# Kernel tuning notes

Measured on AMD Instinct MI355X. Metric: run time of the kernel, lower is better.

## Reference

```python
import jax, jax.numpy as jnp
import numpy as np

V = 30000   # vocab (len(en_dict))
D = 256     # embed/d_model
H = 4       # heads
DK = D // H
N = 1024    # max_len
B = 16      # batch
HID = 256   # ffn hidden
NEG = -1e10
SCALE = 1.0 / np.sqrt(DK)


def setup_inputs() -> dict:
    key = jax.random.key(0)
    ks = jax.random.split(key, 24)
    g = lambda i, shape, s=0.02: jax.random.normal(ks[i], shape, jnp.float32) * s
    return {
        'input_ids': jax.random.randint(ks[0], (B, N), 0, V),
        'attention_mask': jnp.ones((B, N), jnp.int32),
        'emb_W': g(1, (D, V)), 'emb_b': g(2, (D,)),
        'wq': g(3, (D, D)), 'bq': g(4, (D,)),
        'wk': g(5, (D, D)), 'bk': g(6, (D,)),
        'wv': g(7, (D, D)), 'bv': g(8, (D,)),
        'fc_w': g(9, (D, D)), 'fc_b': g(10, (D,)),
        'ff_w1': g(11, (HID, D)), 'ff_b1': g(12, (HID,)),
        'ff_w2': g(13, (D, HID)), 'ff_b2': g(14, (D,)),
        'h1_w': g(15, (128, D)), 'h1_b': g(16, (128,)),
        'bn_gamma': jnp.ones((128,)), 'bn_beta': jnp.zeros((128,)),
        'bn_mean': jnp.zeros((128,)), 'bn_var': jnp.ones((128,)),
        'h2_w': g(17, (1, 128)), 'h2_b': g(18, (1,)),
    }


def _pos_encoding():
    pos = jnp.arange(N, dtype=jnp.float32)[:, None]
    down = jnp.exp(jnp.arange(0, D, 2, dtype=jnp.float32) * (-np.log(10000.0) / D))
    ang = pos * down  # (N, D/2)
    pe = jnp.zeros((N, D), jnp.float32)
    pe = pe.at[:, 0::2].set(jnp.sin(ang) / 10.0)
    pe = pe.at[:, 1::2].set(jnp.cos(ang) / 10.0)
    return pe


def _forward(input_ids, attention_mask, emb_W, emb_b, wq, bq, wk, bk, wv, bv,
             fc_w, fc_b, ff_w1, ff_b1, ff_w2, ff_b2, h1_w, h1_b,
             bn_gamma, bn_beta, bn_mean, bn_var, h2_w, h2_b):
    # one-hot @ W^T + b  ==  direct column gather of W
    x = emb_W.T[input_ids] + emb_b          # (B, N, D)
    x = x + _pos_encoding()                  # dropout off (eval)

    # --- multi-head self-attention with per-sample span mask ---
    def heads(w, b):
        return (jnp.einsum('bnd,ed->bne', x, w) + b).reshape(B, N, H, DK).transpose(0, 2, 1, 3)
    q, k, v = heads(wq, bq), heads(wk, bk), heads(wv, bv)
    scores = jnp.einsum('bhnd,bhmd->bhnm', q, k) * SCALE  # (B,H,N,N)

    m = attention_mask.astype(bool)
    start = jnp.argmax(m, axis=1)                    # first True
    end = N - 1 - jnp.argmax(m[:, ::-1], axis=1)     # last True (exclusive end in slice)
    idx = jnp.arange(N)
    in_span = (idx[None, :] >= start[:, None]) & (idx[None, :] < end[:, None])  # (B,N)
    allowed = in_span[:, :, None] & in_span[:, None, :]                         # (B,N,N)
    scores = scores + jnp.where(allowed, 0.0, NEG)[:, None, :, :]

    p = jax.nn.softmax(scores, axis=-1)
    att = jnp.einsum('bhnm,bhmd->bhnd', p, v).transpose(0, 2, 1, 3).reshape(B, N, D)
    att = jnp.einsum('bnd,ed->bne', att, fc_w) + fc_b
    x = x + att

    # --- feed-forward (replaces x, no residual; dropout off; exact GELU) ---
    h = jax.nn.gelu(jnp.einsum('bnd,hd->bnh', x, ff_w1) + ff_b1, approximate=False)
    x = jnp.einsum('bnh,dh->bnd', h, ff_w2) + ff_b2

    # --- mean pool + MLP head (BatchNorm in eval mode) ---
    pooled = jnp.mean(x, axis=1)                      # (B, D)
    h = pooled @ h1_w.T + h1_b                        # (B, 128)
    h = (h - bn_mean) / jnp.sqrt(bn_var + 1e-5) * bn_gamma + bn_beta
    h = jax.nn.relu(h)
    return h @ h2_w.T + h2_b                          # (B, 1)


def reference(input_ids, attention_mask, emb_W, emb_b, wq, bq, wk, bk, wv, bv,
              fc_w, fc_b, ff_w1, ff_b1, ff_w2, ff_b2, h1_w, h1_b,
              bn_gamma, bn_beta, bn_mean, bn_var, h2_w, h2_b):
    return _forward(input_ids, attention_mask, emb_W, emb_b, wq, bq, wk, bk, wv, bv,
                    fc_w, fc_b, ff_w1, ff_b1, ff_w2, ff_b2, h1_w, h1_b,
                    bn_gamma, bn_beta, bn_mean, bn_var, h2_w, h2_b)
```

## Files before the change

kernel.cpp:

```cpp
#include <hip/hip_runtime.h>
#include <math.h>

#define VOCAB 30000
#define DMODEL 256
#define NHEAD 4
#define SEQ 1024
#define BATCH 16
#define MROWS (BATCH*SEQ)
#define SL2 0.18033688011112042f
#define NEG2 (-1.4426950408889634e10f)

typedef __attribute__((ext_vector_type(8))) short bf16x8;
typedef __attribute__((ext_vector_type(4))) float f32x4;

#if __has_builtin(__builtin_amdgcn_exp2f)
#define EXP2F __builtin_amdgcn_exp2f
#else
#define EXP2F exp2f
#endif

__device__ __forceinline__ unsigned short f2b(float f) {
    unsigned int u = __float_as_uint(f);
    unsigned int r = (u + 0x7FFFu + ((u >> 16) & 1u)) >> 16;
    return (unsigned short)r;
}
__device__ __forceinline__ unsigned short f2b_trunc(float f) {
    return (unsigned short)(__float_as_uint(f) >> 16);
}
__device__ __forceinline__ float b2f(unsigned short s) {
    unsigned int u = ((unsigned int)s) << 16;
    return __uint_as_float(u);
}

__global__ __launch_bounds__(256) void prep_kernel(const int* __restrict__ mask, int* __restrict__ spans,
                                                   float* __restrict__ pe,
                                                   const float* __restrict__ wq, const float* __restrict__ wk,
                                                   const float* __restrict__ wv, const float* __restrict__ bq,
                                                   const float* __restrict__ bk, const float* __restrict__ bv,
                                                   unsigned short* __restrict__ wqkv, float* __restrict__ bias768,
                                                   const float* __restrict__ fcw, const float* __restrict__ f1w,
                                                   const float* __restrict__ f2w, unsigned short* __restrict__ wb3,
                                                   const float* __restrict__ embW, const float* __restrict__ eb,
                                                   unsigned short* __restrict__ embT) {
    int blk = blockIdx.x;
    int t = threadIdx.x;
    if (blk < 64) {
        __shared__ double down[128];
        if (t < 128) down[t] = exp((double)(2 * t) * (-9.210340371976184 / 256.0));
        __syncthreads();
        int d2 = t & 127, half = t >> 7;
        #pragma unroll
        for (int i = 0; i < 8; i++) {
            int n = blk * 16 + half * 8 + i;
            double ang = (double)n * down[d2];
            pe[n * DMODEL + 2 * d2]     = (float)(sin(ang) * 0.1);
            pe[n * DMODEL + 2 * d2 + 1] = (float)(cos(ang) * 0.1);
        }
    } else if (blk < 80) {
        int b = blk - 64;
        __shared__ int smin, smax;
        if (t == 0) { smin = SEQ; smax = -1; }
        __syncthreads();
        int lmin = SEQ, lmax = -1;
        for (int i = t; i < SEQ; i += 256) {
            if (mask[b * SEQ + i] != 0) { lmin = min(lmin, i); lmax = max(lmax, i); }
        }
        atomicMin(&smin, lmin);
        atomicMax(&smax, lmax);
        __syncthreads();
        if (t == 0) {
            int st, en;
            if (smax < 0) { st = 0; en = SEQ - 1; }
            else          { st = smin; en = smax; }
            spans[b * 2] = st; spans[b * 2 + 1] = en;
        }
    } else if (blk < 849) {
        int cb = blk - 80;
        if (cb < 768) {
            const float* src = (cb < 256) ? wq : (cb < 512) ? wk : wv;
            wqkv[cb * 256 + t] = f2b(src[(cb & 255) * 256 + t]);
        } else {
            for (int j = t; j < 768; j += 256)
                bias768[j] = (j < 256) ? bq[j] : (j < 512) ? bk[j - 256] : bv[j - 512];
        }
    } else if (blk < 1617) {
        int cb = blk - 849;
        const float* src = (cb < 256) ? fcw : (cb < 512) ? f1w : f2w;
        wb3[cb * 256 + t] = f2b(src[(cb & 255) * 256 + t]);
    } else {
        __shared__ float tsh[32][33];
        int tb = blk - 1617;
        int bx = tb % 938, by = tb / 938;
        int tx = t & 31, ty = t >> 5;
        int c0 = bx * 32, r0 = by * 32;
        for (int i = 0; i < 32; i += 8) {
            int r = r0 + ty + i, c = c0 + tx;
            if (c < VOCAB) tsh[ty + i][tx] = embW[(size_t)r * VOCAB + c];
        }
        __syncthreads();
        float ebv = eb[r0 + tx];
        for (int i = 0; i < 32; i += 8) {
            int c = c0 + ty + i, r = r0 + tx;
            if (c < VOCAB) embT[(size_t)c * DMODEL + r] = f2b(tsh[tx][ty + i] + ebv);
        }
    }
}

__global__ void embed_kernel(const int* __restrict__ ids, const unsigned short* __restrict__ embT,
                             const float* __restrict__ pe, unsigned short* __restrict__ x0b) {
    int bn = blockIdx.x;
    int d = threadIdx.x;
    int id = ids[bn];
    int n = bn & (SEQ - 1);
    float v = b2f(embT[(size_t)id * DMODEL + d]) + pe[n * DMODEL + d];
    x0b[(size_t)bn * DMODEL + d] = f2b(v);
}

__global__ __launch_bounds__(512) void qkv_kernel(const unsigned short* __restrict__ A,
                                                  const unsigned short* __restrict__ W,
                                                  const float* __restrict__ bias,
                                                  unsigned short* __restrict__ Qb,
                                                  unsigned short* __restrict__ Kb,
                                                  unsigned short* __restrict__ Vt) {
    __shared__ unsigned short XA[4 * 64 * 64];
    __shared__ unsigned short Bs[2][256 * 64];
    int tid = threadIdx.x;
    int m0 = blockIdx.x * 64;
    int w = tid >> 6, l = tid & 63;
    int wrow = w >> 1, wcol = w & 1;
    int lg = l >> 4, ll = l & 15;
    int bb = m0 >> 10;

    #pragma unroll
    for (int i = 0; i < 4; i++) {
        int s = tid + i * 512;
        int row = s >> 5;
        int kb = (s & 31) * 16;
        int kt = kb >> 7, within = kb & 127;
        int swz = within ^ ((row & 7) << 4);
        float4 av = *(const float4*)((const char*)A + (size_t)(m0 + row) * 512 + kb);
        *(float4*)((char*)XA + kt * 8192 + row * 128 + swz) = av;
    }

    for (int nb = 0; nb < 3; nb++) {
        f32x4 acc[8] = {};
        #pragma unroll
        for (int i = 0; i < 4; i++) {
            int s = tid + i * 512;
            int row = s >> 3, kb = (s & 7) * 16;
            int swz = kb ^ ((row & 7) << 4);
            float4 bv = *(const float4*)((const char*)W + (size_t)(nb * 256 + row) * 512 + kb);
            *(float4*)((char*)Bs[0] + row * 128 + swz) = bv;
        }
        __syncthreads();

        for (int kt = 0; kt < 4; kt++) {
            int cur = kt & 1;
            float4 pre[4];
            if (kt < 3) {
                #pragma unroll
                for (int i = 0; i < 4; i++) {
                    int s = tid + i * 512;
                    int row = s >> 3, kb = (s & 7) * 16;
                    pre[i] = *(const float4*)((const char*)W + (size_t)(nb * 256 + row) * 512 + (kt + 1) * 128 + kb);
                }
            }
            int arow = wrow * 16 + ll;
            bf16x8 af[2];
            #pragma unroll
            for (int ks = 0; ks < 2; ks++)
                af[ks] = *(const bf16x8*)((const char*)XA + kt * 8192 + arow * 128 + ((lg * 16 + ks * 64) ^ ((arow & 7) << 4)));
            #pragma unroll
            for (int nf = 0; nf < 8; nf++) {
                int brow = wcol * 128 + nf * 16 + ll;
                #pragma unroll
                for (int ks = 0; ks < 2; ks++) {
                    bf16x8 bf = *(const bf16x8*)((const char*)Bs[cur] + brow * 128 + ((lg * 16 + ks * 64) ^ ((brow & 7) << 4)));
                    acc[nf] = __builtin_amdgcn_mfma_f32_16x16x32_bf16(af[ks], bf, acc[nf], 0, 0, 0);
                }
            }
            if (kt < 3) {
                #pragma unroll
                for (int i = 0; i < 4; i++) {
                    int s = tid + i * 512;
                    int row = s >> 3, kb = (s & 7) * 16;
                    int swz = kb ^ ((row & 7) << 4);
                    *(float4*)((char*)Bs[cur ^ 1] + row * 128 + swz) = pre[i];
                }
            }
            __syncthreads();
        }
        #pragma unroll
        for (int nf = 0; nf < 8; nf++) {
            int col = wcol * 128 + nf * 16 + ll;
            float bv = bias[nb * 256 + col];
            int hh = col >> 6, dk = col & 63;
            if (nb == 2) {
                unsigned int lo = (unsigned int)f2b(acc[nf][0] + bv) | ((unsigned int)f2b(acc[nf][1] + bv) << 16);
                unsigned int hi = (unsigned int)f2b(acc[nf][2] + bv) | ((unsigned int)f2b(acc[nf][3] + bv) << 16);
                int ns = (m0 & 1023) + wrow * 16 + lg * 4;
                unsigned int* dst = (unsigned int*)(Vt + ((((size_t)bb * 4 + hh) * 64) + dk) * 1024 + ns);
                dst[0] = lo;
                dst[1] = hi;
            } else {
                #pragma unroll
                for (int r2 = 0; r2 < 4; r2++) {
                    int ns = (m0 & 1023) + wrow * 16 + lg * 4 + r2;
                    float v = acc[nf][r2] + bv;
                    if (nb == 0)
                        Qb[((((size_t)bb * 4 + hh) * 1024) + ns) * 64 + dk] = f2b(v * SL2);
                    else
                        Kb[((((size_t)bb * 4 + hh) * 1024) + ns) * 64 + dk] = f2b(v);
                }
            }
        }
    }
}

__global__ __launch_bounds__(512) void attn_coop(const unsigned short* __restrict__ Qb,
                                                 const unsigned short* __restrict__ Kb,
                                                 const unsigned short* __restrict__ Vt,
                                                 const int* __restrict__ spans,
                                                 unsigned short* __restrict__ attb) {
    __shared__ unsigned short Ks[2][64 * 64];
    __shared__ unsigned short Vs[2][64 * 64];
    __shared__ __align__(16) unsigned short Ps[8][16 * 72];
    int tid = threadIdx.x;
    int w = tid >> 6, l = tid & 63;
    int id = blockIdx.x;
    int c = id & 7, rest = id >> 3;
    int bh = c * 8 + (rest >> 3);
    int qg = rest & 7;
    int q0 = qg * 128 + w * 16;
    int b = bh >> 2, h = bh & 3;
    int lg = l >> 4, ll = l & 15;
    const char* Kp = (const char*)(Kb + (size_t)bh * SEQ * 64);
    const char* Vp = (const char*)(Vt + (size_t)bh * 64 * SEQ);
    const unsigned short* Qp = Qb + (size_t)bh * SEQ * 64;
    int start = spans[b * 2], end = spans[b * 2 + 1];

    bf16x8 qf[2];
    #pragma unroll
    for (int ks = 0; ks < 2; ks++)
        qf[ks] = *(const bf16x8*)(Qp + (size_t)(q0 + ll) * 64 + lg * 8 + ks * 32);

    bf16x8 ones;
    #pragma unroll
    for (int i = 0; i < 8; i++) ones[i] = (short)0x3F80;

    f32x4 o[4] = {};
    f32x4 accl = {};
    bool rowok[4];
    #pragma unroll
    for (int r2 = 0; r2 < 4; r2++) {
        int rr = q0 + lg * 4 + r2;
        rowok[r2] = (rr >= start) && (rr < end);
    }

    int srow = tid >> 3, skb = (tid & 7) * 16;
    int sswz = skb ^ ((srow & 7) << 4);

    {
        float4 kv0v = *(const float4*)(Kp + (size_t)srow * 128 + skb);
        float4 vv0 = *(const float4*)(Vp + (size_t)srow * 2048 + skb);
        *(float4*)((char*)Ks[0] + srow * 128 + sswz) = kv0v;
        *(float4*)((char*)Vs[0] + srow * 128 + sswz) = vv0;
    }

    for (int ct = 0; ct < 16; ct++) {
        int cur = ct & 1;
        int kv0 = ct * 64;
        __syncthreads();

        float4 kreg, vreg;
        if (ct < 15) {
            int kvn = kv0 + 64;
            kreg = *(const float4*)(Kp + (size_t)(kvn + srow) * 128 + skb);
            vreg = *(const float4*)(Vp + (size_t)srow * 2048 + kvn * 2 + skb);
        }

        f32x4 s4[4];
        #pragma unroll
        for (int nf = 0; nf < 4; nf++) {
            int cc = kv0 + nf * 16 + ll;
            float ci = ((cc >= start) && (cc < end)) ? 0.f : NEG2;
            f32x4 cv = { ci, ci, ci, ci };
            s4[nf] = cv;
        }
        #pragma unroll
        for (int ks = 0; ks < 2; ks++)
            #pragma unroll
            for (int nf = 0; nf < 4; nf++) {
                int row = nf * 16 + ll;
                bf16x8 kf = *(const bf16x8*)((const char*)Ks[cur] + row * 128 + ((lg * 16 + ks * 64) ^ ((row & 7) << 4)));
                s4[nf] = __builtin_amdgcn_mfma_f32_16x16x32_bf16(qf[ks], kf, s4[nf], 0, 0, 0);
            }

        #pragma unroll
        for (int nf = 0; nf < 4; nf++)
            #pragma unroll
            for (int r2 = 0; r2 < 4; r2++) {
                float sv = rowok[r2] ? s4[nf][r2] : 0.f;
                s4[nf][r2] = EXP2F(sv);
            }

        #pragma unroll
        for (int nf = 0; nf < 4; nf++)
            #pragma unroll
            for (int r2 = 0; r2 < 4; r2++)
                Ps[w][(lg * 4 + r2) * 72 + nf * 16 + ll] = f2b_trunc(s4[nf][r2]);

        bf16x8 pa[2];
        #pragma unroll
        for (int ks = 0; ks < 2; ks++)
            pa[ks] = *(const bf16x8*)(&Ps[w][ll * 72 + lg * 8 + ks * 32]);

        #pragma unroll
        for (int ks = 0; ks < 2; ks++)
            #pragma unroll
            for (int cf = 0; cf < 4; cf++) {
                int row = cf * 16 + ll;
                bf16x8 vf = *(const bf16x8*)((const char*)Vs[cur] + row * 128 + ((lg * 16 + ks * 64) ^ ((row & 7) << 4)));
                o[cf] = __builtin_amdgcn_mfma_f32_16x16x32_bf16(pa[ks], vf, o[cf], 0, 0, 0);
            }
        #pragma unroll
        for (int ks = 0; ks < 2; ks++)
            accl = __builtin_amdgcn_mfma_f32_16x16x32_bf16(pa[ks], ones, accl, 0, 0, 0);

        if (ct < 15) {
            *(float4*)((char*)Ks[cur ^ 1] + srow * 128 + sswz) = kreg;
            *(float4*)((char*)Vs[cur ^ 1] + srow * 128 + sswz) = vreg;
        }
    }

    #pragma unroll
    for (int r2 = 0; r2 < 4; r2++) {
        float inv = 1.f / accl[r2];
        int row = q0 + lg * 4 + r2;
        #pragma unroll
        for (int cf = 0; cf < 4; cf++) {
            int dk = cf * 16 + ll;
            attb[((size_t)b * SEQ + row) * 256 + h * 64 + dk] = f2b(o[cf][r2] * inv);
        }
    }
}

__global__ __launch_bounds__(512) void ffn_kernel(const unsigned short* __restrict__ attb,
                                                  const unsigned short* __restrict__ x0b,
                                                  const unsigned short* __restrict__ W3,
                                                  const float* __restrict__ fcb,
                                                  const float* __restrict__ f1b,
                                                  const float* __restrict__ f2bv,
                                                  float* __restrict__ part) {
    __shared__ unsigned short BufA[4 * 64 * 64];
    __shared__ unsigned short BufB[4 * 64 * 64];
    __shared__ unsigned short Bs[2][256 * 64];
    int tid = threadIdx.x;
    int m0 = blockIdx.x * 64;
    int w = tid >> 6, l = tid & 63;
    int wrow = w >> 1, wcol = w & 1;
    int lg = l >> 4, ll = l & 15;
    int arow = wrow * 16 + ll;

    #pragma unroll
    for (int i = 0; i < 4; i++) {
        int s = tid + i * 512;
        int row = s >> 5;
        int kb = (s & 31) * 16;
        int kt = kb >> 7, within = kb & 127;
        int swz = within ^ ((row & 7) << 4);
        float4 av = *(const float4*)((const char*)attb + (size_t)(m0 + row) * 512 + kb);
        *(float4*)((char*)BufA + kt * 8192 + row * 128 + swz) = av;
    }

    #pragma unroll
    for (int phase = 0; phase < 3; phase++) {
        const unsigned short* Wp = W3 + phase * 65536;
        const char* Asrc = (phase == 1) ? (const char*)BufB : (const char*)BufA;
        f32x4 acc[8] = {};
        #pragma unroll
        for (int i = 0; i < 4; i++) {
            int s = tid + i * 512;
            int row = s >> 3, kb = (s & 7) * 16;
            int swz = kb ^ ((row & 7) << 4);
            float4 bv = *(const float4*)((const char*)Wp + (size_t)row * 512 + kb);
            *(float4*)((char*)Bs[0] + row * 128 + swz) = bv;
        }
        __syncthreads();

        for (int kt = 0; kt < 4; kt++) {
            int cur = kt & 1;
            float4 pre[4];
            if (kt < 3) {
                #pragma unroll
                for (int i = 0; i < 4; i++) {
                    int s = tid + i * 512;
                    int row = s >> 3, kb = (s & 7) * 16;
                    pre[i] = *(const float4*)((const char*)Wp + (size_t)row * 512 + (kt + 1) * 128 + kb);
                }
            }
            bf16x8 af[2];
            #pragma unroll
            for (int ks = 0; ks < 2; ks++)
                af[ks] = *(const bf16x8*)(Asrc + kt * 8192 + arow * 128 + ((lg * 16 + ks * 64) ^ ((arow & 7) << 4)));
            #pragma unroll
            for (int nf = 0; nf < 8; nf++) {
                int brow = wcol * 128 + nf * 16 + ll;
                #pragma unroll
                for (int ks = 0; ks < 2; ks++) {
                    bf16x8 bf = *(const bf16x8*)((const char*)Bs[cur] + brow * 128 + ((lg * 16 + ks * 64) ^ ((brow & 7) << 4)));
                    acc[nf] = __builtin_amdgcn_mfma_f32_16x16x32_bf16(af[ks], bf, acc[nf], 0, 0, 0);
                }
            }
            if (kt < 3) {
                #pragma unroll
                for (int i = 0; i < 4; i++) {
                    int s = tid + i * 512;
                    int row = s >> 3, kb = (s & 7) * 16;
                    int swz = kb ^ ((row & 7) << 4);
                    *(float4*)((char*)Bs[cur ^ 1] + row * 128 + swz) = pre[i];
                }
            }
            __syncthreads();
        }

        if (phase == 0) {
            #pragma unroll
            for (int nf = 0; nf < 8; nf++) {
                int col = wcol * 128 + nf * 16 + ll;
                float bv = fcb[col];
                int kt = col >> 6;
                int byteoff = (2 * (col & 63));
                #pragma unroll
                for (int r2 = 0; r2 < 4; r2++) {
                    int row = wrow * 16 + lg * 4 + r2;
                    *(unsigned short*)((char*)BufB + kt * 8192 + row * 128 + (byteoff ^ ((row & 7) << 4))) = f2b(acc[nf][r2] + bv);
                }
            }
            __syncthreads();
            #pragma unroll
            for (int i = 0; i < 4; i++) {
                int s = tid + i * 512;
                int row = s >> 5;
                int kb = (s & 31) * 16;
                int kt = kb >> 7, within = kb & 127;
                int swz = within ^ ((row & 7) << 4);
                bf16x8* dst = (bf16x8*)((char*)BufB + kt * 8192 + row * 128 + swz);
                bf16x8 xv = *dst;
                bf16x8 rv = *(const bf16x8*)((const char*)x0b + (size_t)(m0 + row) * 512 + kb);
                bf16x8 res;
                #pragma unroll
                for (int jj = 0; jj < 8; jj++)
                    res[jj] = (short)f2b(b2f((unsigned short)xv[jj]) + b2f((unsigned short)rv[jj]));
                *dst = res;
            }
        } else if (phase == 1) {
            #pragma unroll
            for (int nf = 0; nf < 8; nf++) {
                int col = wcol * 128 + nf * 16 + ll;
                float bv = f1b[col];
                int kt = col >> 6;
                int byteoff = (2 * (col & 63));
                #pragma unroll
                for (int r2 = 0; r2 < 4; r2++) {
                    int row = wrow * 16 + lg * 4 + r2;
                    float v = acc[nf][r2] + bv;
                    v = 0.5f * v * (1.f + erff(v * 0.70710678118654752f));
                    *(unsigned short*)((char*)BufA + kt * 8192 + row * 128 + (byteoff ^ ((row & 7) << 4))) = f2b(v);
                }
            }
        } else {
            int bb = m0 >> 10;
            int chunk = ((m0 & 1023) >> 4) + wrow;
            #pragma unroll
            for (int nf = 0; nf < 8; nf++) {
                int col = wcol * 128 + nf * 16 + ll;
                float s_ = acc[nf][0] + acc[nf][1] + acc[nf][2] + acc[nf][3];
                s_ += __shfl_xor(s_, 16);
                s_ += __shfl_xor(s_, 32);
                s_ += 16.f * f2bv[col];
                if (lg == 0)
                    part[((size_t)bb * 64 + chunk) * 256 + col] = s_;
            }
        }
    }
}

__global__ __launch_bounds__(128) void head2_kernel(const float* __restrict__ part,
                                                    const float* __restrict__ h1_w, const float* __restrict__ h1_b,
                                                    const float* __restrict__ g, const float* __restrict__ be,
                                                    const float* __restrict__ mu, const float* __restrict__ var,
                                                    const float* __restrict__ h2_w, const float* __restrict__ h2_b,
                                                    float* __restrict__ out) {
    int b = blockIdx.x, j = threadIdx.x;
    __shared__ float pl[256];
    __shared__ float red[128];
    float s0 = 0.f, s1 = 0.f;
    for (int ch = 0; ch < 64; ch++) {
        s0 += part[((size_t)b * 64 + ch) * 256 + j];
        s1 += part[((size_t)b * 64 + ch) * 256 + j + 128];
    }
    pl[j] = s0 * (1.f / 1024.f);
    pl[j + 128] = s1 * (1.f / 1024.f);
    __syncthreads();
    float s = 0.f;
    for (int d = 0; d < 256; d++) s = fmaf(pl[d], h1_w[j * 256 + d], s);
    s += h1_b[j];
    s = (s - mu[j]) / sqrtf(var[j] + 1e-5f) * g[j] + be[j];
    s = fmaxf(s, 0.f);
    red[j] = s * h2_w[j];
    __syncthreads();
    for (int off = 64; off; off >>= 1) {
        if (j < off) red[j] += red[j + off];
        __syncthreads();
    }
    if (j == 0) out[b] = red[0] + h2_b[0];
}

extern "C" void kernel_launch(void* const* d_in, const int* in_sizes, int n_in,
                              void* d_out, int out_size, void* d_ws, size_t ws_size,
                              hipStream_t stream) {
    (void)in_sizes; (void)n_in; (void)out_size; (void)ws_size;
    const int*   ids    = (const int*)d_in[0];
    const int*   amask  = (const int*)d_in[1];
    const float* emb_W  = (const float*)d_in[2];
    const float* emb_b  = (const float*)d_in[3];
    const float* wq = (const float*)d_in[4],  *bq = (const float*)d_in[5];
    const float* wk = (const float*)d_in[6],  *bk = (const float*)d_in[7];
    const float* wv = (const float*)d_in[8],  *bv = (const float*)d_in[9];
    const float* fcw = (const float*)d_in[10], *fcb = (const float*)d_in[11];
    const float* f1w = (const float*)d_in[12], *f1b = (const float*)d_in[13];
    const float* f2w = (const float*)d_in[14], *f2b_ = (const float*)d_in[15];
    const float* h1w = (const float*)d_in[16], *h1b = (const float*)d_in[17];
    const float* bng = (const float*)d_in[18], *bnb = (const float*)d_in[19];
    const float* bnm = (const float*)d_in[20], *bnv = (const float*)d_in[21];
    const float* h2w = (const float*)d_in[22], *h2b = (const float*)d_in[23];
    float* out = (float*)d_out;
    float* ws = (float*)d_ws;

    const size_t O_PE   = 0;
    const size_t O_EMBT = O_PE + 262144;
    const size_t O_X0B  = O_EMBT + 3840000;
    const size_t O_Q    = O_X0B + 2097152;
    const size_t O_K    = O_Q + 2097152;
    const size_t O_V    = O_K + 2097152;
    const size_t O_ATT  = O_V + 2097152;
    const size_t O_WQKV = O_ATT + 2097152;
    const size_t O_WB3  = O_WQKV + 98304;
    const size_t O_B768 = O_WB3 + 98304;
    const size_t O_PART = O_B768 + 768;
    const size_t O_SPAN = O_PART + 262144;

    float* pe   = ws + O_PE;
    unsigned short* embT = (unsigned short*)(ws + O_EMBT);
    unsigned short* x0b  = (unsigned short*)(ws + O_X0B);
    unsigned short* Qb   = (unsigned short*)(ws + O_Q);
    unsigned short* Kb   = (unsigned short*)(ws + O_K);
    unsigned short* Vt   = (unsigned short*)(ws + O_V);
    unsigned short* attb = (unsigned short*)(ws + O_ATT);
    unsigned short* wqkv = (unsigned short*)(ws + O_WQKV);
    unsigned short* wb3  = (unsigned short*)(ws + O_WB3);
    float* bias768 = ws + O_B768;
    float* part = ws + O_PART;
    int* spans  = (int*)(ws + O_SPAN);

    prep_kernel<<<1617 + 938 * 8, 256, 0, stream>>>(amask, spans, pe,
                                                    wq, wk, wv, bq, bk, bv, wqkv, bias768,
                                                    fcw, f1w, f2w, wb3,
                                                    emb_W, emb_b, embT);
    embed_kernel<<<MROWS, 256, 0, stream>>>(ids, embT, pe, x0b);

    qkv_kernel<<<256, 512, 0, stream>>>(x0b, wqkv, bias768, Qb, Kb, Vt);

    attn_coop<<<512, 512, 0, stream>>>(Qb, Kb, Vt, spans, attb);

    ffn_kernel<<<256, 512, 0, stream>>>(attb, x0b, wb3, fcb, f1b, f2b_, part);

    head2_kernel<<<BATCH, 128, 0, stream>>>(part, h1w, h1b, bng, bnb, bnm, bnv, h2w, h2b, out);
}
```

Before: 100.1 us.

## Fuse embedding gather into QKV kernel and retile FFN to 32-row blocks

Removes the separate embed kernel by gathering embedding rows and adding positional encoding inside the QKV kernel's A-tile load, also writing x0b for the residual. The FFN kernel is retiled from 64-row to 32-row blocks with 4 column-warps, doubling the grid to 512 blocks, and drops the double-buffered weight tile in favour of a single buffer with extra barriers. This saves a launch and a round trip of x0b, and gives more FFN blocks for occupancy, at the cost of reloading the weights twice as often and losing load/compute overlap in the FFN.

```diff
diff --git a/kernel.cpp b/kernel.cpp
--- a/kernel.cpp
+++ b/kernel.cpp
@@ -106,19 +106,12 @@
     }
 }
 
-__global__ void embed_kernel(const int* __restrict__ ids, const unsigned short* __restrict__ embT,
-                             const float* __restrict__ pe, unsigned short* __restrict__ x0b) {
-    int bn = blockIdx.x;
-    int d = threadIdx.x;
-    int id = ids[bn];
-    int n = bn & (SEQ - 1);
-    float v = b2f(embT[(size_t)id * DMODEL + d]) + pe[n * DMODEL + d];
-    x0b[(size_t)bn * DMODEL + d] = f2b(v);
-}
-
-__global__ __launch_bounds__(512) void qkv_kernel(const unsigned short* __restrict__ A,
+__global__ __launch_bounds__(512) void qkv_kernel(const int* __restrict__ ids,
+                                                  const unsigned short* __restrict__ embT,
+                                                  const float* __restrict__ pe,
                                                   const unsigned short* __restrict__ W,
                                                   const float* __restrict__ bias,
+                                                  unsigned short* __restrict__ x0b,
                                                   unsigned short* __restrict__ Qb,
                                                   unsigned short* __restrict__ Kb,
                                                   unsigned short* __restrict__ Vt) {
@@ -138,8 +131,23 @@
         int kb = (s & 31) * 16;
         int kt = kb >> 7, within = kb & 127;
         int swz = within ^ ((row & 7) << 4);
-        float4 av = *(const float4*)((const char*)A + (size_t)(m0 + row) * 512 + kb);
-        *(float4*)((char*)XA + kt * 8192 + row * 128 + swz) = av;
+        int tok = m0 + row;
+        int id = ids[tok];
+        int n = tok & (SEQ - 1);
+        bf16x8 ev = *(const bf16x8*)((const char*)embT + (size_t)id * 512 + kb);
+        float4 p0 = *(const float4*)((const char*)pe + (size_t)n * 1024 + kb * 2);
+        float4 p1 = *(const float4*)((const char*)pe + (size_t)n * 1024 + kb * 2 + 16);
+        bf16x8 xv;
+        xv[0] = (short)f2b(b2f((unsigned short)ev[0]) + p0.x);
+        xv[1] = (short)f2b(b2f((unsigned short)ev[1]) + p0.y);
+        xv[2] = (short)f2b(b2f((unsigned short)ev[2]) + p0.z);
+        xv[3] = (short)f2b(b2f((unsigned short)ev[3]) + p0.w);
+        xv[4] = (short)f2b(b2f((unsigned short)ev[4]) + p1.x);
+        xv[5] = (short)f2b(b2f((unsigned short)ev[5]) + p1.y);
+        xv[6] = (short)f2b(b2f((unsigned short)ev[6]) + p1.z);
+        xv[7] = (short)f2b(b2f((unsigned short)ev[7]) + p1.w);
+        *(bf16x8*)((char*)XA + kt * 8192 + row * 128 + swz) = xv;
+        *(bf16x8*)((char*)x0b + (size_t)tok * 512 + kb) = xv;
     }
 
     for (int nb = 0; nb < 3; nb++) {
@@ -352,100 +360,88 @@
                                                   const float* __restrict__ f1b,
                                                   const float* __restrict__ f2bv,
                                                   float* __restrict__ part) {
-    __shared__ unsigned short BufA[4 * 64 * 64];
-    __shared__ unsigned short BufB[4 * 64 * 64];
-    __shared__ unsigned short Bs[2][256 * 64];
+    __shared__ unsigned short BufA[4 * 32 * 64];
+    __shared__ unsigned short BufB[4 * 32 * 64];
+    __shared__ unsigned short Bs[256 * 64];
     int tid = threadIdx.x;
-    int m0 = blockIdx.x * 64;
+    int m0 = blockIdx.x * 32;
     int w = tid >> 6, l = tid & 63;
-    int wrow = w >> 1, wcol = w & 1;
+    int wrow = w >> 2, wcol = w & 3;
     int lg = l >> 4, ll = l & 15;
     int arow = wrow * 16 + ll;
 
     #pragma unroll
-    for (int i = 0; i < 4; i++) {
+    for (int i = 0; i < 2; i++) {
         int s = tid + i * 512;
         int row = s >> 5;
         int kb = (s & 31) * 16;
         int kt = kb >> 7, within = kb & 127;
         int swz = within ^ ((row & 7) << 4);
         float4 av = *(const float4*)((const char*)attb + (size_t)(m0 + row) * 512 + kb);
-        *(float4*)((char*)BufA + kt * 8192 + row * 128 + swz) = av;
+        *(float4*)((char*)BufA + kt * 4096 + row * 128 + swz) = av;
     }
 
     #pragma unroll
     for (int phase = 0; phase < 3; phase++) {
         const unsigned short* Wp = W3 + phase * 65536;
         const char* Asrc = (phase == 1) ? (const char*)BufB : (const char*)BufA;
-        f32x4 acc[8] = {};
-        #pragma unroll
-        for (int i = 0; i < 4; i++) {
-            int s = tid + i * 512;
-            int row = s >> 3, kb = (s & 7) * 16;
-            int swz = kb ^ ((row & 7) << 4);
-            float4 bv = *(const float4*)((const char*)Wp + (size_t)row * 512 + kb);
-            *(float4*)((char*)Bs[0] + row * 128 + swz) = bv;
-        }
-        __syncthreads();
+        f32x4 acc[4] = {};
 
         for (int kt = 0; kt < 4; kt++) {
-            int cur = kt & 1;
             float4 pre[4];
-            if (kt < 3) {
-                #pragma unroll
-                for (int i = 0; i < 4; i++) {
-                    int s = tid + i * 512;
-                    int row = s >> 3, kb = (s & 7) * 16;
-                    pre[i] = *(const float4*)((const char*)Wp + (size_t)row * 512 + (kt + 1) * 128 + kb);
-                }
-            }
+            #pragma unroll
+            for (int i = 0; i < 4; i++) {
+                int s = tid + i * 512;
+                int row = s >> 3, kb = (s & 7) * 16;
+                pre[i] = *(const float4*)((const char*)Wp + (size_t)row * 512 + kt * 128 + kb);
+            }
+            __syncthreads();
+            #pragma unroll
+            for (int i = 0; i < 4; i++) {
+                int s = tid + i * 512;
+                int row = s >> 3, kb = (s & 7) * 16;
+                int swz = kb ^ ((row & 7) << 4);
+                *(float4*)((char*)Bs + row * 128 + swz) = pre[i];
+            }
+            __syncthreads();
             bf16x8 af[2];
             #pragma unroll
             for (int ks = 0; ks < 2; ks++)
-                af[ks] = *(const bf16x8*)(Asrc + kt * 8192 + arow * 128 + ((lg * 16 + ks * 64) ^ ((arow & 7) << 4)));
-            #pragma unroll
-            for (int nf = 0; nf < 8; nf++) {
-                int brow = wcol * 128 + nf * 16 + ll;
+                af[ks] = *(const bf16x8*)(Asrc + kt * 4096 + arow * 128 + ((lg * 16 + ks * 64) ^ ((arow & 7) << 4)));
+            #pragma unroll
+            for (int nf = 0; nf < 4; nf++) {
+                int brow = wcol * 64 + nf * 16 + ll;
                 #pragma unroll
                 for (int ks = 0; ks < 2; ks++) {
-                    bf16x8 bf = *(const bf16x8*)((const char*)Bs[cur] + brow * 128 + ((lg * 16 + ks * 64) ^ ((brow & 7) << 4)));
+                    bf16x8 bf = *(const bf16x8*)((const char*)Bs + brow * 128 + ((lg * 16 + ks * 64) ^ ((brow & 7) << 4)));
                     acc[nf] = __builtin_amdgcn_mfma_f32_16x16x32_bf16(af[ks], bf, acc[nf], 0, 0, 0);
                 }
             }
-            if (kt < 3) {
-                #pragma unroll
-                for (int i = 0; i < 4; i++) {
-                    int s = tid + i * 512;
-                    int row = s >> 3, kb = (s & 7) * 16;
-                    int swz = kb ^ ((row & 7) << 4);
-                    *(float4*)((char*)Bs[cur ^ 1] + row * 128 + swz) = pre[i];
-                }
-            }
+        }
+
+        if (phase == 0) {
             __syncthreads();
-        }
-
-        if (phase == 0) {
-            #pragma unroll
-            for (int nf = 0; nf < 8; nf++) {
-                int col = wcol * 128 + nf * 16 + ll;
+            #pragma unroll
+            for (int nf = 0; nf < 4; nf++) {
+                int col = wcol * 64 + nf * 16 + ll;
                 float bv = fcb[col];
                 int kt = col >> 6;
                 int byteoff = (2 * (col & 63));
                 #pragma unroll
                 for (int r2 = 0; r2 < 4; r2++) {
                     int row = wrow * 16 + lg * 4 + r2;
-                    *(unsigned short*)((char*)BufB + kt * 8192 + row * 128 + (byteoff ^ ((row & 7) << 4))) = f2b(acc[nf][r2] + bv);
+                    *(unsigned short*)((char*)BufB + kt * 4096 + row * 128 + (byteoff ^ ((row & 7) << 4))) = f2b(acc[nf][r2] + bv);
                 }
             }
             __syncthreads();
             #pragma unroll
-            for (int i = 0; i < 4; i++) {
+            for (int i = 0; i < 2; i++) {
                 int s = tid + i * 512;
                 int row = s >> 5;
                 int kb = (s & 31) * 16;
                 int kt = kb >> 7, within = kb & 127;
                 int swz = within ^ ((row & 7) << 4);
-                bf16x8* dst = (bf16x8*)((char*)BufB + kt * 8192 + row * 128 + swz);
+                bf16x8* dst = (bf16x8*)((char*)BufB + kt * 4096 + row * 128 + swz);
                 bf16x8 xv = *dst;
                 bf16x8 rv = *(const bf16x8*)((const char*)x0b + (size_t)(m0 + row) * 512 + kb);
                 bf16x8 res;
@@ -455,9 +451,10 @@
                 *dst = res;
             }
         } else if (phase == 1) {
-            #pragma unroll
-            for (int nf = 0; nf < 8; nf++) {
-                int col = wcol * 128 + nf * 16 + ll;
+            __syncthreads();
+            #pragma unroll
+            for (int nf = 0; nf < 4; nf++) {
+                int col = wcol * 64 + nf * 16 + ll;
                 float bv = f1b[col];
                 int kt = col >> 6;
                 int byteoff = (2 * (col & 63));
@@ -466,15 +463,15 @@
                     int row = wrow * 16 + lg * 4 + r2;
                     float v = acc[nf][r2] + bv;
                     v = 0.5f * v * (1.f + erff(v * 0.70710678118654752f));
-                    *(unsigned short*)((char*)BufA + kt * 8192 + row * 128 + (byteoff ^ ((row & 7) << 4))) = f2b(v);
+                    *(unsigned short*)((char*)BufA + kt * 4096 + row * 128 + (byteoff ^ ((row & 7) << 4))) = f2b(v);
                 }
             }
         } else {
             int bb = m0 >> 10;
-            int chunk = ((m0 & 1023) >> 4) + wrow;
-            #pragma unroll
-            for (int nf = 0; nf < 8; nf++) {
-                int col = wcol * 128 + nf * 16 + ll;
+            int chunk = ((m0 & 1023) >> 5) * 2 + wrow;
+            #pragma unroll
+            for (int nf = 0; nf < 4; nf++) {
+                int col = wcol * 64 + nf * 16 + ll;
                 float s_ = acc[nf][0] + acc[nf][1] + acc[nf][2] + acc[nf][3];
                 s_ += __shfl_xor(s_, 16);
                 s_ += __shfl_xor(s_, 32);
@@ -568,13 +565,12 @@
                                                     wq, wk, wv, bq, bk, bv, wqkv, bias768,
                                                     fcw, f1w, f2w, wb3,
                                                     emb_W, emb_b, embT);
-    embed_kernel<<<MROWS, 256, 0, stream>>>(ids, embT, pe, x0b);
-
-    qkv_kernel<<<256, 512, 0, stream>>>(x0b, wqkv, bias768, Qb, Kb, Vt);
+
+    qkv_kernel<<<256, 512, 0, stream>>>(ids, embT, pe, wqkv, bias768, x0b, Qb, Kb, Vt);
 
     attn_coop<<<512, 512, 0, stream>>>(Qb, Kb, Vt, spans, attb);
 
-    ffn_kernel<<<256, 512, 0, stream>>>(attb, x0b, wb3, fcb, f1b, f2b_, part);
+    ffn_kernel<<<512, 512, 0, stream>>>(attb, x0b, wb3, fcb, f1b, f2b_, part);
 
     head2_kernel<<<BATCH, 128, 0, stream>>>(part, h1w, h1b, bng, bnb, bnm, bnv, h2w, h2b, out);
 }
```

New measurement: 138.6 us. +38.4%, slower.
